# Kernel tuning notes

Measured on AMD Instinct MI355X. Metric: run time of the kernel, lower is better.

The kernel has to match this reference:

```python
import jax, jax.numpy as jnp
import numpy as np

DIM = 768
NUM_HEADS = 12
HEAD_DIM = DIM // NUM_HEADS
SCALE = HEAD_DIM ** -0.5
B, N = 8, 1024


def setup_inputs() -> dict:
    key = jax.random.key(0)
    k1, k2, k3, k4 = jax.random.split(key, 4)
    s = 1.0 / np.sqrt(DIM)
    return {
        "x": jax.random.normal(k1, (B, N, DIM), dtype=jnp.float32),
        "w_qkv": jax.random.normal(k2, (DIM, 3 * DIM), dtype=jnp.float32) * s,  # qkv_bias=False
        "w_proj": jax.random.normal(k3, (DIM, DIM), dtype=jnp.float32) * s,
        "b_proj": jax.random.normal(k4, (DIM,), dtype=jnp.float32) * 0.01,
    }


def reference(x, w_qkv, w_proj, b_proj):
    Bb, Nn, C = x.shape
    qkv = x @ w_qkv  # [B, N, 3C]
    qkv = qkv.reshape(Bb, Nn, 3, NUM_HEADS, HEAD_DIM)
    q = qkv[:, :, 0].transpose(0, 2, 1, 3)  # [B, H, N, d]
    k = qkv[:, :, 1].transpose(0, 2, 1, 3)
    v = qkv[:, :, 2].transpose(0, 2, 1, 3)
    attn = jnp.einsum("bhqd,bhkd->bhqk", q, k) * SCALE
    attn = jax.nn.softmax(attn, axis=-1)  # dropout p=0 -> identity
    out = jnp.einsum("bhqk,bhkd->bhqd", attn, v)
    out = out.transpose(0, 2, 1, 3).reshape(Bb, Nn, C)
    return out @ w_proj + b_proj
```

## Files before the change

kernel.cpp:

```cpp
#include <hip/hip_runtime.h>
#include <stdint.h>

typedef __attribute__((ext_vector_type(8))) __bf16 bf16x8;
typedef __attribute__((ext_vector_type(8))) unsigned short u16x8;
typedef __attribute__((ext_vector_type(4))) unsigned short u16x4;
typedef __attribute__((ext_vector_type(4))) short s16x4;
typedef __attribute__((ext_vector_type(4))) float f32x4;

typedef unsigned int u32_as1 __attribute__((address_space(1)));
typedef unsigned int u32_as3 __attribute__((address_space(3)));

__device__ __forceinline__ unsigned short f2bf(float f) {
  unsigned int u = __float_as_uint(f);
  u += 0x7fffu + ((u >> 16) & 1u);
  return (unsigned short)(u >> 16);
}

__device__ __forceinline__ bf16x8 ld_frag(const unsigned short* p) {
  return __builtin_bit_cast(bf16x8, *(const u16x8*)p);
}

__device__ __forceinline__ f32x4 mfma16(s16x4 a, s16x4 b, f32x4 c) {
#if __has_builtin(__builtin_amdgcn_mfma_f32_16x16x16bf16_1k)
  return __builtin_amdgcn_mfma_f32_16x16x16bf16_1k(a, b, c, 0, 0, 0);
#elif __has_builtin(__builtin_amdgcn_mfma_f32_16x16x16_bf16_1k)
  return __builtin_amdgcn_mfma_f32_16x16x16_bf16_1k(a, b, c, 0, 0, 0);
#else
  asm volatile("v_mfma_f32_16x16x16_bf16 %0, %1, %2, %0"
               : "+v"(c) : "v"(a), "v"(b));
  return c;
#endif
}

__device__ __forceinline__ float fast_exp2(float x) {
#if __has_builtin(__builtin_amdgcn_exp2f)
  return __builtin_amdgcn_exp2f(x);
#else
  return exp2f(x);
#endif
}

__device__ __forceinline__ void async16(const void* g, void* l) {
  const u32_as1* gp = (const u32_as1*)(uintptr_t)g;
  u32_as3* lp = (u32_as3*)(uintptr_t)l;
  __builtin_amdgcn_global_load_lds(gp, lp, 16, 0, 0);
}

__global__ __launch_bounds__(256) void convert_bf16(const float4* __restrict__ in,
                                                    u16x4* __restrict__ out, int n4) {
  int i = blockIdx.x * 256 + threadIdx.x;
  if (i < n4) {
    float4 v = in[i];
    u16x4 o;
    o[0] = f2bf(v.x); o[1] = f2bf(v.y); o[2] = f2bf(v.z); o[3] = f2bf(v.w);
    out[i] = o;
  }
}

__global__ __launch_bounds__(256) void transpose_bf16(const float* __restrict__ w,
                                                      unsigned short* __restrict__ wt,
                                                      int K, int N) {
  __shared__ float tile[32][33];
  const int n0 = blockIdx.x * 32, k0 = blockIdx.y * 32;
  const int tx = threadIdx.x, ty = threadIdx.y;
#pragma unroll
  for (int r = 0; r < 4; r++)
    tile[ty + r * 8][tx] = w[(k0 + ty + r * 8) * N + n0 + tx];
  __syncthreads();
#pragma unroll
  for (int r = 0; r < 4; r++)
    wt[(n0 + ty + r * 8) * K + k0 + tx] = f2bf(tile[tx][ty + r * 8]);
}

template <int EPI>
__global__ __launch_bounds__(256, 2) void gemm_bt(
    const unsigned short* __restrict__ A, const unsigned short* __restrict__ Bt,
    unsigned short* __restrict__ qb, unsigned short* __restrict__ kb,
    unsigned short* __restrict__ vtb, float* __restrict__ outp,
    const float* __restrict__ bias) {
  __shared__ unsigned short As[128 * 32];
  __shared__ unsigned short Bs[128 * 32];
  const int t = threadIdx.x;
  const int lane = t & 63, w = t >> 6;
  const int quad = lane >> 4, l15 = lane & 15;
  const int m0 = blockIdx.y * 128, n0 = blockIdx.x * 128;
  const int wm = (w & 1) * 64, wn = (w >> 1) * 64;

  f32x4 acc[4][4];
  const f32x4 fzero = {0.f, 0.f, 0.f, 0.f};
#pragma unroll
  for (int i = 0; i < 4; i++)
#pragma unroll
    for (int j = 0; j < 4; j++) acc[i][j] = fzero;

  const int srow = w * 16 + (lane >> 2);
  const int scol = (lane & 3) * 8;
  const unsigned short* Ag = A + (m0 + srow) * 768 + scol;
  const unsigned short* Bg = Bt + (n0 + srow) * 768 + scol;
  unsigned short* Asl = As + w * 512 + lane * 8;
  unsigned short* Bsl = Bs + w * 512 + lane * 8;

  for (int k0 = 0; k0 < 768; k0 += 32) {
    __syncthreads();
    async16(Ag + k0, Asl);
    async16(Ag + 64 * 768 + k0, Asl + 2048);
    async16(Bg + k0, Bsl);
    async16(Bg + 64 * 768 + k0, Bsl + 2048);
    __syncthreads();

    bf16x8 af[4], bfr[4];
#pragma unroll
    for (int i = 0; i < 4; i++)
      af[i] = ld_frag(As + (wm + i * 16 + l15) * 32 + quad * 8);
#pragma unroll
    for (int j = 0; j < 4; j++)
      bfr[j] = ld_frag(Bs + (wn + j * 16 + l15) * 32 + quad * 8);
#pragma unroll
    for (int i = 0; i < 4; i++)
#pragma unroll
      for (int j = 0; j < 4; j++)
        acc[i][j] = __builtin_amdgcn_mfma_f32_16x16x32_bf16(af[i], bfr[j], acc[i][j], 0, 0, 0);
  }

#pragma unroll
  for (int i = 0; i < 4; i++) {
    const int gmb = m0 + wm + i * 16 + quad * 4;
#pragma unroll
    for (int j = 0; j < 4; j++) {
      const int gc = n0 + wn + j * 16 + l15;
#pragma unroll
      for (int r = 0; r < 4; r++) {
        const int gm = gmb + r;
        float v = acc[i][j][r];
        if (EPI == 0) {
          const int b = gm >> 10, tok = gm & 1023;
          const int which = (gc >= 1536) ? 2 : (gc >= 768 ? 1 : 0);
          const int rem = gc - which * 768;
          const int h = rem >> 6, d = rem & 63;
          const int bh = b * 12 + h;
          const unsigned short bv = f2bf(v);
          if (which == 0)      qb[(bh << 16) + (tok << 6) + d] = bv;
          else if (which == 1) kb[(bh << 16) + (tok << 6) + d] = bv;
          else                 vtb[(bh << 16) + (d << 10) + tok] = bv;
        } else {
          outp[gm * 768 + gc] = v + bias[gc];
        }
      }
    }
  }
}

#define SWZC(row, c) (((row) << 6) + ((((c) + (row)) & 7) << 3))
#define C2 0.1803368801111244f

__global__ __launch_bounds__(256, 3) void attn_kernel(
    const unsigned short* __restrict__ qb, const unsigned short* __restrict__ kb,
    const unsigned short* __restrict__ vtb, unsigned short* __restrict__ aout) {
  __shared__ unsigned short smem[9216];
  unsigned short* Ks = smem;
  unsigned short* Vts = smem + 4096;

  const int t = threadIdx.x;
  const int lane = t & 63, w = t >> 6;
  const int quad = lane >> 4, l15 = lane & 15;
  const int bh = blockIdx.x;
  const int b = bh / 12, h = bh - b * 12;
  const int q0 = blockIdx.y * 128;
  const int base = bh << 16;

  bf16x8 qf[2][2];
#pragma unroll
  for (int qt = 0; qt < 2; qt++)
#pragma unroll
    for (int s = 0; s < 2; s++)
      qf[qt][s] = ld_frag(qb + base + ((q0 + w * 32 + qt * 16 + l15) << 6) +
                          s * 32 + quad * 8);

  f32x4 oacc[4][2];
  const f32x4 fzero = {0.f, 0.f, 0.f, 0.f};
#pragma unroll
  for (int dt = 0; dt < 4; dt++) { oacc[dt][0] = fzero; oacc[dt][1] = fzero; }
  float lsum0 = 0.f, lsum1 = 0.f;

  const int srow = t >> 3, schk = t & 7;
  const int c0 = ((schk - srow) & 7) * 8;
  const int c1 = ((schk - (srow + 32)) & 7) * 8;

  for (int kv0 = 0; kv0 < 1024; kv0 += 64) {
    __syncthreads();
    async16(kb + base + ((kv0 + srow) << 6) + c0, Ks + t * 8);
    async16(kb + base + ((kv0 + srow + 32) << 6) + c1, Ks + 2048 + t * 8);
    async16(vtb + base + (srow << 10) + kv0 + c0, Vts + t * 8);
    async16(vtb + base + ((srow + 32) << 10) + kv0 + c1, Vts + 2048 + t * 8);
    __syncthreads();

    f32x4 st[4][2];
#pragma unroll
    for (int tc = 0; tc < 4; tc++) { st[tc][0] = fzero; st[tc][1] = fzero; }
#pragma unroll
    for (int s = 0; s < 2; s++) {
#pragma unroll
      for (int tc = 0; tc < 4; tc++) {
        const bf16x8 kf = ld_frag(Ks + SWZC(tc * 16 + l15, s * 4 + quad));
        st[tc][0] = __builtin_amdgcn_mfma_f32_16x16x32_bf16(kf, qf[0][s], st[tc][0], 0, 0, 0);
        st[tc][1] = __builtin_amdgcn_mfma_f32_16x16x32_bf16(kf, qf[1][s], st[tc][1], 0, 0, 0);
      }
    }

    s16x4 pf[4][2];
#pragma unroll
    for (int tc = 0; tc < 4; tc++) {
#pragma unroll
      for (int qt = 0; qt < 2; qt++) {
        const float p0 = fast_exp2(st[tc][qt][0] * C2);
        const float p1 = fast_exp2(st[tc][qt][1] * C2);
        const float p2 = fast_exp2(st[tc][qt][2] * C2);
        const float p3 = fast_exp2(st[tc][qt][3] * C2);
        const float ps = (p0 + p1) + (p2 + p3);
        if (qt == 0) lsum0 += ps; else lsum1 += ps;
        s16x4 pk;
        pk[0] = (short)f2bf(p0); pk[1] = (short)f2bf(p1);
        pk[2] = (short)f2bf(p2); pk[3] = (short)f2bf(p3);
        pf[tc][qt] = pk;
      }
    }

#pragma unroll
    for (int tc = 0; tc < 4; tc++) {
#pragma unroll
      for (int dt = 0; dt < 4; dt++) {
        const int row = dt * 16 + l15;
        const int addr = (row << 6) + ((((tc * 2 + (quad >> 1)) + row) & 7) << 3) +
                         ((quad & 1) << 2);
        const s16x4 vf = *(const s16x4*)(Vts + addr);
        oacc[dt][0] = mfma16(vf, pf[tc][0], oacc[dt][0]);
        oacc[dt][1] = mfma16(vf, pf[tc][1], oacc[dt][1]);
      }
    }
  }

  lsum0 += __shfl_xor(lsum0, 16); lsum0 += __shfl_xor(lsum0, 32);
  lsum1 += __shfl_xor(lsum1, 16); lsum1 += __shfl_xor(lsum1, 32);
  const float inv0 = 1.f / lsum0, inv1 = 1.f / lsum1;

  __syncthreads();
  unsigned short* Ot = smem;
#pragma unroll
  for (int dt = 0; dt < 4; dt++) {
#pragma unroll
    for (int qt = 0; qt < 2; qt++) {
      const float inv = qt == 0 ? inv0 : inv1;
      const int qrow = (w * 32 + qt * 16 + l15) * 72 + dt * 16 + quad * 4;
#pragma unroll
      for (int r = 0; r < 4; r++)
        Ot[qrow + r] = f2bf(oacc[dt][qt][r] * inv);
    }
  }
  __syncthreads();
#pragma unroll
  for (int it = 0; it < 4; it++) {
    const int q = it * 32 + (t >> 3);
    const int d0 = (t & 7) * 8;
    const u16x8 v = *(const u16x8*)(Ot + q * 72 + d0);
    *(u16x8*)(aout + (b * 1024 + q0 + q) * 768 + h * 64 + d0) = v;
  }
}

extern "C" void kernel_launch(void* const* d_in, const int* in_sizes, int n_in,
                              void* d_out, int out_size, void* d_ws, size_t ws_size,
                              hipStream_t stream) {
  (void)in_sizes; (void)n_in; (void)out_size; (void)ws_size;
  const float* x = (const float*)d_in[0];
  const float* w_qkv = (const float*)d_in[1];
  const float* w_proj = (const float*)d_in[2];
  const float* b_proj = (const float*)d_in[3];
  float* out = (float*)d_out;

  char* ws = (char*)d_ws;
  unsigned short* x_bf   = (unsigned short*)(ws);
  unsigned short* wqkvT  = (unsigned short*)(ws + 12582912);
  unsigned short* wprojT = (unsigned short*)(ws + 16121856);
  unsigned short* qb     = (unsigned short*)(ws + 17301504);
  unsigned short* kb     = (unsigned short*)(ws + 29884416);
  unsigned short* vtb    = (unsigned short*)(ws + 42467328);
  unsigned short* aout   = x_bf;

  convert_bf16<<<6144, 256, 0, stream>>>((const float4*)x, (u16x4*)x_bf, 1572864);
  transpose_bf16<<<dim3(72, 24), dim3(32, 8), 0, stream>>>(w_qkv, wqkvT, 768, 2304);
  transpose_bf16<<<dim3(24, 24), dim3(32, 8), 0, stream>>>(w_proj, wprojT, 768, 768);
  gemm_bt<0><<<dim3(18, 64), 256, 0, stream>>>(x_bf, wqkvT, qb, kb, vtb, nullptr, nullptr);
  attn_kernel<<<dim3(96, 8), 256, 0, stream>>>(qb, kb, vtb, aout);
  gemm_bt<1><<<dim3(6, 64), 256, 0, stream>>>(aout, wprojT, nullptr, nullptr, nullptr, out, b_proj);
}
```

Measured before the change: 214.0 us.

## Merge prep kernels, swizzle GEMM LDS, remap blocks per XCD, smaller proj tiles

Folds the x conversion and both weight transposes into a single prep launch, removing two launches. The GEMM now XOR-style rotates the k-chunk placement in LDS to reduce bank conflicts on fragment reads. It also maps block IDs so that the blocks on each XCD share M rows for L2 reuse. The tile width is now a template parameter, and the projection GEMM uses 128x64 tiles (768 blocks instead of 384) to fill more CUs, with launch bounds raised to 4 waves/SIMD, which may pressure registers.

```diff
diff --git a/kernel.cpp b/kernel.cpp
--- a/kernel.cpp
+++ b/kernel.cpp
@@ -46,55 +46,62 @@
   __builtin_amdgcn_global_load_lds(gp, lp, 16, 0, 0);
 }
 
-__global__ __launch_bounds__(256) void convert_bf16(const float4* __restrict__ in,
-                                                    u16x4* __restrict__ out, int n4) {
-  int i = blockIdx.x * 256 + threadIdx.x;
-  if (i < n4) {
-    float4 v = in[i];
+__global__ __launch_bounds__(256) void prep_kernel(
+    const float* __restrict__ x, const float* __restrict__ w_qkv,
+    const float* __restrict__ w_proj, u16x4* __restrict__ x_bf,
+    unsigned short* __restrict__ wqkvT, unsigned short* __restrict__ wprojT) {
+  const int bid = blockIdx.x;
+  const int t = threadIdx.x;
+  if (bid < 6144) {
+    const int i = bid * 256 + t;
+    float4 v = ((const float4*)x)[i];
     u16x4 o;
     o[0] = f2bf(v.x); o[1] = f2bf(v.y); o[2] = f2bf(v.z); o[3] = f2bf(v.w);
-    out[i] = o;
-  }
-}
-
-__global__ __launch_bounds__(256) void transpose_bf16(const float* __restrict__ w,
-                                                      unsigned short* __restrict__ wt,
-                                                      int K, int N) {
+    x_bf[i] = o;
+    return;
+  }
   __shared__ float tile[32][33];
-  const int n0 = blockIdx.x * 32, k0 = blockIdx.y * 32;
-  const int tx = threadIdx.x, ty = threadIdx.y;
+  const float* w; unsigned short* wt; int N, bx, by;
+  if (bid < 6144 + 1728) { const int r = bid - 6144; w = w_qkv; wt = wqkvT; N = 2304; bx = r % 72; by = r / 72; }
+  else                   { const int r = bid - 7872; w = w_proj; wt = wprojT; N = 768; bx = r % 24; by = r / 24; }
+  const int n0 = bx * 32, k0 = by * 32;
+  const int tx = t & 31, ty = t >> 5;
 #pragma unroll
   for (int r = 0; r < 4; r++)
     tile[ty + r * 8][tx] = w[(k0 + ty + r * 8) * N + n0 + tx];
   __syncthreads();
 #pragma unroll
   for (int r = 0; r < 4; r++)
-    wt[(n0 + ty + r * 8) * K + k0 + tx] = f2bf(tile[tx][ty + r * 8]);
-}
-
-template <int EPI>
-__global__ __launch_bounds__(256, 2) void gemm_bt(
+    wt[(n0 + ty + r * 8) * 768 + k0 + tx] = f2bf(tile[tx][ty + r * 8]);
+}
+
+template <int EPI, int NT, int NBLK>
+__global__ __launch_bounds__(256, 4) void gemm_bt(
     const unsigned short* __restrict__ A, const unsigned short* __restrict__ Bt,
     unsigned short* __restrict__ qb, unsigned short* __restrict__ kb,
     unsigned short* __restrict__ vtb, float* __restrict__ outp,
     const float* __restrict__ bias) {
   __shared__ unsigned short As[128 * 32];
-  __shared__ unsigned short Bs[128 * 32];
+  __shared__ unsigned short Bs[NT * 64 * 32];
   const int t = threadIdx.x;
   const int lane = t & 63, w = t >> 6;
   const int quad = lane >> 4, l15 = lane & 15;
-  const int m0 = blockIdx.y * 128, n0 = blockIdx.x * 128;
-  const int wm = (w & 1) * 64, wn = (w >> 1) * 64;
-
-  f32x4 acc[4][4];
+
+  const int bid = blockIdx.x;
+  const int xcd = bid & 7, slot = bid >> 3;
+  const int m0 = (xcd * 8 + slot / NBLK) * 128;
+  const int n0 = (slot % NBLK) * (NT * 64);
+  const int wm = (w & 1) * 64, wn = (w >> 1) * (NT * 32);
+
+  f32x4 acc[4][NT * 2];
   const f32x4 fzero = {0.f, 0.f, 0.f, 0.f};
 #pragma unroll
   for (int i = 0; i < 4; i++)
 #pragma unroll
-    for (int j = 0; j < 4; j++) acc[i][j] = fzero;
+    for (int j = 0; j < NT * 2; j++) acc[i][j] = fzero;
 
   const int srow = w * 16 + (lane >> 2);
-  const int scol = (lane & 3) * 8;
+  const int scol = (((lane & 3) - (srow >> 1)) & 3) * 8;
   const unsigned short* Ag = A + (m0 + srow) * 768 + scol;
   const unsigned short* Bg = Bt + (n0 + srow) * 768 + scol;
   unsigned short* Asl = As + w * 512 + lane * 8;
@@ -104,21 +111,26 @@
     __syncthreads();
     async16(Ag + k0, Asl);
     async16(Ag + 64 * 768 + k0, Asl + 2048);
-    async16(Bg + k0, Bsl);
-    async16(Bg + 64 * 768 + k0, Bsl + 2048);
+#pragma unroll
+    for (int f = 0; f < NT; f++)
+      async16(Bg + f * 64 * 768 + k0, Bsl + f * 2048);
     __syncthreads();
 
-    bf16x8 af[4], bfr[4];
+    bf16x8 af[4], bfr[NT * 2];
+#pragma unroll
+    for (int i = 0; i < 4; i++) {
+      const int row = wm + i * 16 + l15;
+      af[i] = ld_frag(As + row * 32 + (((quad + (row >> 1)) & 3) << 3));
+    }
+#pragma unroll
+    for (int j = 0; j < NT * 2; j++) {
+      const int row = wn + j * 16 + l15;
+      bfr[j] = ld_frag(Bs + row * 32 + (((quad + (row >> 1)) & 3) << 3));
+    }
 #pragma unroll
     for (int i = 0; i < 4; i++)
-      af[i] = ld_frag(As + (wm + i * 16 + l15) * 32 + quad * 8);
-#pragma unroll
-    for (int j = 0; j < 4; j++)
-      bfr[j] = ld_frag(Bs + (wn + j * 16 + l15) * 32 + quad * 8);
-#pragma unroll
-    for (int i = 0; i < 4; i++)
-#pragma unroll
-      for (int j = 0; j < 4; j++)
+#pragma unroll
+      for (int j = 0; j < NT * 2; j++)
         acc[i][j] = __builtin_amdgcn_mfma_f32_16x16x32_bf16(af[i], bfr[j], acc[i][j], 0, 0, 0);
   }
 
@@ -126,7 +138,7 @@
   for (int i = 0; i < 4; i++) {
     const int gmb = m0 + wm + i * 16 + quad * 4;
 #pragma unroll
-    for (int j = 0; j < 4; j++) {
+    for (int j = 0; j < NT * 2; j++) {
       const int gc = n0 + wn + j * 16 + l15;
 #pragma unroll
       for (int r = 0; r < 4; r++) {
@@ -285,10 +297,8 @@
   unsigned short* vtb    = (unsigned short*)(ws + 42467328);
   unsigned short* aout   = x_bf;
 
-  convert_bf16<<<6144, 256, 0, stream>>>((const float4*)x, (u16x4*)x_bf, 1572864);
-  transpose_bf16<<<dim3(72, 24), dim3(32, 8), 0, stream>>>(w_qkv, wqkvT, 768, 2304);
-  transpose_bf16<<<dim3(24, 24), dim3(32, 8), 0, stream>>>(w_proj, wprojT, 768, 768);
-  gemm_bt<0><<<dim3(18, 64), 256, 0, stream>>>(x_bf, wqkvT, qb, kb, vtb, nullptr, nullptr);
+  prep_kernel<<<8448, 256, 0, stream>>>(x, w_qkv, w_proj, (u16x4*)x_bf, wqkvT, wprojT);
+  gemm_bt<0, 2, 18><<<1152, 256, 0, stream>>>(x_bf, wqkvT, qb, kb, vtb, nullptr, nullptr);
   attn_kernel<<<dim3(96, 8), 256, 0, stream>>>(qb, kb, vtb, aout);
-  gemm_bt<1><<<dim3(6, 64), 256, 0, stream>>>(aout, wprojT, nullptr, nullptr, nullptr, out, b_proj);
-}
+  gemm_bt<1, 1, 12><<<768, 256, 0, stream>>>(aout, wprojT, nullptr, nullptr, nullptr, out, b_proj);
+}
```

Result: no change. 211.1 us (-1.4%).
